# Optimization experiments

Measured on AMD Instinct MI355X. Metric: run time of the kernel, lower is better.

Reference implementation:

```python
import jax, jax.numpy as jnp
import numpy as np

B, N, E, H = 4, 2048, 256, 8
D = E // H
EPS = 1e-5


def _layernorm(x, g, b):
    mu = jnp.mean(x, axis=-1, keepdims=True)
    var = jnp.mean(jnp.square(x - mu), axis=-1, keepdims=True)
    return (x - mu) * jax.lax.rsqrt(var + EPS) * g + b


def setup_inputs() -> dict:
    key = jax.random.key(0)
    ks = jax.random.split(key, 8)
    s = 1.0 / np.sqrt(E)
    lin = lambda k: (jax.random.normal(k, (E, E), jnp.float32) * s)
    return {
        "x_l": jax.random.normal(ks[0], (B, N, E), jnp.float32),
        "x_r": jax.random.normal(ks[1], (B, N, E), jnp.float32),
        "Wq": lin(ks[2]), "bq": jnp.zeros((E,), jnp.float32),
        "Wk": lin(ks[3]), "bk": jnp.zeros((E,), jnp.float32),
        "Wv": lin(ks[4]), "bv": jnp.zeros((E,), jnp.float32),
        "Wp": lin(ks[5]), "bp": jnp.zeros((E,), jnp.float32),
        "ln_g": jnp.ones((E,), jnp.float32), "ln_b": jnp.zeros((E,), jnp.float32),
        "rn_g": jnp.ones((E,), jnp.float32), "rn_b": jnp.zeros((E,), jnp.float32),
    }


def reference(x_l, x_r, Wq, bq, Wk, bk, Wv, bv, Wp, bp, ln_g, ln_b, rn_g, rn_b):
    # projections -> [b, h, n, d]
    q = (x_l @ Wq + bq).reshape(B, N, H, D).transpose(0, 2, 1, 3)
    k = (x_r @ Wk + bk).reshape(B, N, H, D).transpose(0, 2, 1, 3)
    # shared value from the difference of the two streams
    v = ((x_l - x_r) @ Wv + bv).reshape(B, N, H, D).transpose(0, 2, 1, 3)

    energy = jnp.einsum('bhqd,bhkd->bhqk', q, k)  # [b,h,n,n]
    attn = jax.nn.softmax(energy / np.sqrt(D), axis=-1)  # dropout p=0 (eval)

    # attn used as-is and transposed against the SAME value tensor
    out_l = jnp.einsum('bhqk,bhkd->bhqd', attn, v)
    out_r = jnp.einsum('bhqk,bhqd->bhkd', attn, v)  # == attn^T @ v

    out_l = out_l.transpose(0, 2, 1, 3).reshape(B, N, E)
    out_r = out_r.transpose(0, 2, 1, 3).reshape(B, N, E)

    out_l = _layernorm(out_l @ Wp + bp, ln_g, ln_b) + x_l
    out_r = _layernorm(out_r @ Wp + bp, rn_g, rn_b) + x_r
    return (out_l, out_r)
```

## Files before the change

kernel.cpp:

```cpp
#include <hip/hip_runtime.h>
#include <math.h>


typedef __attribute__((ext_vector_type(8))) short short8;
typedef __attribute__((ext_vector_type(4))) float f32x4;
typedef __attribute__((ext_vector_type(16))) float f32x16;
typedef __attribute__((ext_vector_type(4))) unsigned short u16x4;

union FragU { unsigned int u[4]; short8 s8; };

__device__ __forceinline__ unsigned short bf16_rn(float f) {
    union { float f; unsigned int u; } c; c.f = f;
    return (unsigned short)((c.u + 0x7FFFu + ((c.u >> 16) & 1u)) >> 16);
}
__device__ __forceinline__ float b2f(unsigned short u) {
    union { unsigned int i; float f; } c; c.i = ((unsigned int)u) << 16;
    return c.f;
}

#if __has_builtin(__builtin_amdgcn_exp2f)
__device__ __forceinline__ float fexp2(float x) { return __builtin_amdgcn_exp2f(x); }
#else
__device__ __forceinline__ float fexp2(float x) { return exp2f(x); }
#endif

__device__ __forceinline__ f32x4 mfma16(short8 a, short8 b, f32x4 c) {
    return __builtin_amdgcn_mfma_f32_16x16x32_bf16(a, b, c, 0, 0, 0);
}
__device__ __forceinline__ f32x16 mfma32(short8 a, short8 b, f32x16 c) {
    return __builtin_amdgcn_mfma_f32_32x32x16_bf16(a, b, c, 0, 0, 0);
}

__device__ __forceinline__ void plswap(unsigned int& x, unsigned int& y) {
    asm("v_permlane32_swap_b32 %0, %1" : "+v"(x), "+v"(y));
}

__device__ __forceinline__ short8 pfrag(unsigned int w0, unsigned int w1,
                                        unsigned int w2, unsigned int w3) {
    plswap(w0, w2);
    plswap(w1, w3);
    FragU fu;
    fu.u[0] = w0; fu.u[1] = w1; fu.u[2] = w2; fu.u[3] = w3;
    return fu.s8;
}

__global__ void prep_all(const float* __restrict__ xl, const float* __restrict__ xr,
                         const float* __restrict__ Wq, const float* __restrict__ Wk,
                         const float* __restrict__ Wv, const float* __restrict__ Wp,
                         unsigned short* __restrict__ xlb, unsigned short* __restrict__ xrb,
                         unsigned short* __restrict__ xdb,
                         unsigned short* __restrict__ Wqt, unsigned short* __restrict__ Wkt,
                         unsigned short* __restrict__ Wvt, unsigned short* __restrict__ Wpt) {
    const int bid = blockIdx.x;
    if (bid < 2048) {
        const size_t i = ((size_t)bid * 256 + threadIdx.x) * 4;
        const float4 A = *(const float4*)(xl + i);
        const float4 Bv = *(const float4*)(xr + i);
        u16x4 pa = { bf16_rn(A.x), bf16_rn(A.y), bf16_rn(A.z), bf16_rn(A.w) };
        u16x4 pb = { bf16_rn(Bv.x), bf16_rn(Bv.y), bf16_rn(Bv.z), bf16_rn(Bv.w) };
        u16x4 pd = { bf16_rn(A.x - Bv.x), bf16_rn(A.y - Bv.y),
                     bf16_rn(A.z - Bv.z), bf16_rn(A.w - Bv.w) };
        *(u16x4*)(xlb + i) = pa;
        *(u16x4*)(xrb + i) = pb;
        *(u16x4*)(xdb + i) = pd;
    } else {
        const int gid = (bid - 2048) * 256 + threadIdx.x;
        const int m = gid >> 16;
        const int idx = gid & 65535;
        const int k = idx >> 8, n = idx & 255;
        const float* W = (m == 0) ? Wq : (m == 1) ? Wk : (m == 2) ? Wv : Wp;
        unsigned short* Wt = (m == 0) ? Wqt : (m == 1) ? Wkt : (m == 2) ? Wvt : Wpt;
        Wt[n * 256 + k] = bf16_rn(W[(size_t)k * 256 + n]);
    }
}

__launch_bounds__(256)
__global__ void qkv_gemm(const unsigned short* __restrict__ xlb,
                         const unsigned short* __restrict__ xrb,
                         const unsigned short* __restrict__ xdb,
                         const unsigned short* __restrict__ Wqt,
                         const unsigned short* __restrict__ Wkt,
                         const unsigned short* __restrict__ Wvt,
                         const float* __restrict__ bq, const float* __restrict__ bk,
                         const float* __restrict__ bv,
                         unsigned short* __restrict__ Qg, unsigned short* __restrict__ Kg,
                         unsigned short* __restrict__ Vtg) {
    const int z = blockIdx.z;
    const unsigned short* A  = (z == 0) ? xlb : (z == 1) ? xrb : xdb;
    const unsigned short* Wt = (z == 0) ? Wqt : (z == 1) ? Wkt : Wvt;
    const float* bias        = (z == 0) ? bq  : (z == 1) ? bk  : bv;

    __shared__ unsigned short At[2][128][40];
    __shared__ unsigned short Bt[2][64][40];

    const int tid = threadIdx.x;
    const int lane = tid & 63, wv = tid >> 6;
    const int a = lane & 15, g = lane >> 4;
    const int wr = wv >> 1, wc = wv & 1;
    const int r0 = blockIdx.x * 128;
    const int c0 = blockIdx.y * 64;

    const f32x4 fz = {0.f, 0.f, 0.f, 0.f};
    f32x4 acc[4][2];
#pragma unroll
    for (int f = 0; f < 4; ++f)
#pragma unroll
        for (int t = 0; t < 2; ++t) acc[f][t] = fz;

    const int arow = tid >> 1, aoff = (tid & 1) * 16;
    const int brow = tid >> 2, boff = (tid & 3) * 8;
    const unsigned short* asrc = A + (size_t)(r0 + arow) * 256 + aoff;
    const unsigned short* bsrc = Wt + (size_t)(c0 + brow) * 256 + boff;

#define QKV_STAGE(KS, BUF)                                                      \
    {                                                                           \
        *(short8*)&At[BUF][arow][aoff]     = *(const short8*)(asrc + (KS) * 32); \
        *(short8*)&At[BUF][arow][aoff + 8] = *(const short8*)(asrc + (KS) * 32 + 8); \
        *(short8*)&Bt[BUF][brow][boff]     = *(const short8*)(bsrc + (KS) * 32); \
    }

    QKV_STAGE(0, 0)
    __syncthreads();

#pragma unroll
    for (int ks = 0; ks < 8; ++ks) {
        const int b = ks & 1;
        if (ks < 7) QKV_STAGE(ks + 1, b ^ 1)
        short8 af[4], bfr[2];
#pragma unroll
        for (int f = 0; f < 4; ++f) af[f] = *(const short8*)&At[b][wr * 64 + f * 16 + a][g * 8];
#pragma unroll
        for (int t = 0; t < 2; ++t) bfr[t] = *(const short8*)&Bt[b][wc * 32 + t * 16 + a][g * 8];
#pragma unroll
        for (int f = 0; f < 4; ++f)
#pragma unroll
            for (int t = 0; t < 2; ++t) acc[f][t] = mfma16(af[f], bfr[t], acc[f][t]);
        __syncthreads();
    }
#undef QKV_STAGE

    const float scq = 0.17677669529663687f * 1.4426950408889634f;
#pragma unroll
    for (int t = 0; t < 2; ++t) {
        const int C = c0 + wc * 32 + t * 16 + a;
        const float bb = bias[C];
        const int h = C >> 5, d = C & 31;
#pragma unroll
        for (int f = 0; f < 4; ++f) {
            const int Rb = r0 + wr * 64 + f * 16 + g * 4;
            const int b_ = Rb >> 11, n = Rb & 2047;
            const int bhh = b_ * 8 + h;
            float v[4];
#pragma unroll
            for (int r = 0; r < 4; ++r) {
                v[r] = acc[f][t][r] + bb;
                if (z == 0) v[r] *= scq;
            }
            if (z < 2) {
                unsigned short* dst = ((z == 0) ? Qg : Kg) + (size_t)(bhh * 2048 + n) * 32 + d;
#pragma unroll
                for (int r = 0; r < 4; ++r) dst[(size_t)r * 32] = bf16_rn(v[r]);
            } else {
                u16x4 pk = { bf16_rn(v[0]), bf16_rn(v[1]), bf16_rn(v[2]), bf16_rn(v[3]) };
                *(u16x4*)(Vtg + (size_t)(bhh * 32 + d) * 2048 + n) = pk;
            }
        }
    }
}

#define P1_TILE(SB)                                                             \
    {                                                                           \
        const short8 ck0 = *(const short8*)((SB) + ro);                         \
        const short8 ck1 = *(const short8*)((SB) + 512 + ro);                   \
        const short8 cv0 = *(const short8*)((SB) + 1024 + ro);                  \
        const short8 cv1 = *(const short8*)((SB) + 1536 + ro);                  \
        f32x16 s = {};                                                          \
        s = mfma32(ck0, qf0, s);                                                \
        s = mfma32(ck1, qf1, s);                                                \
        float p[16];                                                            \
        _Pragma("unroll") for (int j = 0; j < 16; ++j) p[j] = fexp2(s[j]);      \
        l_run += (((p[0] + p[1]) + (p[2] + p[3])) + ((p[4] + p[5]) + (p[6] + p[7]))) \
               + (((p[8] + p[9]) + (p[10] + p[11])) + ((p[12] + p[13]) + (p[14] + p[15]))); \
        unsigned int w[8];                                                      \
        _Pragma("unroll") for (int mm = 0; mm < 8; ++mm)                        \
            asm("v_cvt_pk_bf16_f32 %0, %1, %2"                                  \
                : "=v"(w[mm]) : "v"(p[2 * mm]), "v"(p[2 * mm + 1]));            \
        acc = mfma32(cv0, pfrag(w[0], w[1], w[2], w[3]), acc);                  \
        acc = mfma32(cv1, pfrag(w[4], w[5], w[6], w[7]), acc);                  \
    }

__launch_bounds__(512, 4)
__global__ void attn_pass1(const unsigned short* __restrict__ Qg,
                           const unsigned short* __restrict__ Kg,
                           const unsigned short* __restrict__ Vtg,
                           unsigned short* __restrict__ AOl,
                           unsigned short* __restrict__ Vsg) {
    __shared__ unsigned short ST[2][2][2][2][2][64][8];
    __shared__ float lsumS[4][64];

    float (*accS)[16][64] = (float (*)[16][64])&ST[0][0][0][0][0][0][0];

    const int f = blockIdx.x;
    const int bh = 4 * (f & 7) + (f >> 7);
    const int qblk = (f >> 3) & 15;
    const int tid = threadIdx.x;
    const int wv = tid >> 6;
    const int qi = wv & 3, z = wv >> 2;
    const int lane = tid & 63, l31 = lane & 31, hi = lane >> 5;
    const int q0 = qblk * 128 + qi * 32;

    const unsigned short* Qb = Qg + (size_t)bh * 2048 * 32;
    const unsigned short* Kb = Kg + (size_t)bh * 2048 * 32;
    const unsigned short* Vb = Vtg + (size_t)bh * 32 * 2048;

    const short8 qf0 = *(const short8*)(Qb + (size_t)(q0 + l31) * 32 + hi * 8);
    const short8 qf1 = *(const short8*)(Qb + (size_t)(q0 + l31) * 32 + 16 + hi * 8);

    const int kv = qi >> 1;
    const int srow = (qi & 1) * 16 + (lane >> 2);
    const int m = lane & 3;
    unsigned short* wp00 = &ST[z][0][0][kv][m >> 1][srow + 32 * (m & 1)][0];
    unsigned short* wp01 = &ST[z][0][1][kv][m >> 1][srow + 32 * (m & 1)][0];
    unsigned short* wp10 = &ST[z][1][0][kv][m >> 1][srow + 32 * (m & 1)][0];
    unsigned short* wp11 = &ST[z][1][1][kv][m >> 1][srow + 32 * (m & 1)][0];
    const size_t gstep = kv ? 32 : 1024;
    const unsigned short* sgb = kv
        ? Vb + (size_t)srow * 2048 + m * 8
        : Kb + (size_t)srow * 32 + m * 8;
    const int zt = z * 32;

    const unsigned short* rb00 = &ST[z][0][0][0][0][0][0];
    const unsigned short* rb01 = &ST[z][0][1][0][0][0][0];
    const unsigned short* rb10 = &ST[z][1][0][0][0][0][0];
    const unsigned short* rb11 = &ST[z][1][1][0][0][0][0];
    const int ro = (l31 + 32 * hi) * 8;

    f32x16 acc = {};
    float l_run = 0.f;

    short8 rr0 = *(const short8*)(sgb + (size_t)(zt + 0) * gstep);
    short8 rr1 = *(const short8*)(sgb + (size_t)(zt + 1) * gstep);
    *(short8*)wp00 = rr0;
    *(short8*)wp01 = rr1;
    rr0 = *(const short8*)(sgb + (size_t)(zt + 2) * gstep);
    rr1 = *(const short8*)(sgb + (size_t)(zt + 3) * gstep);
    __syncthreads();

#pragma unroll
    for (int ph = 0; ph < 16; ++ph) {
        const int pb = ph & 1;
        unsigned short* wA = pb ? wp00 : wp10;
        unsigned short* wB = pb ? wp01 : wp11;
        const unsigned short* rA = pb ? rb10 : rb00;
        const unsigned short* rB = pb ? rb11 : rb01;
        if (ph < 15) { *(short8*)wA = rr0; *(short8*)wB = rr1; }
        if (ph < 14) {
            rr0 = *(const short8*)(sgb + (size_t)(zt + 2 * ph + 4) * gstep);
            rr1 = *(const short8*)(sgb + (size_t)(zt + 2 * ph + 5) * gstep);
        }
        P1_TILE(rA)
        P1_TILE(rB)
        __syncthreads();
    }

    float lsum = l_run + __shfl_xor(l_run, 32);

    if (z == 1) {
#pragma unroll
        for (int j = 0; j < 16; ++j) accS[qi][j][lane] = acc[j];
        lsumS[qi][lane] = lsum;
    }
    __syncthreads();
    if (z == 0) {
        lsum += lsumS[qi][lane];
        const float rl = 1.0f / lsum;
#pragma unroll
        for (int j = 0; j < 16; ++j) acc[j] += accS[qi][j][lane];

        const int b_ = bh >> 3, h = bh & 7;
        const int q = q0 + l31;
        unsigned short* dst = AOl + (size_t)(b_ * 2048 + q) * 256 + h * 32;
#pragma unroll
        for (int g2 = 0; g2 < 4; ++g2) {
            u16x4 pk = { bf16_rn(acc[4 * g2 + 0] * rl), bf16_rn(acc[4 * g2 + 1] * rl),
                         bf16_rn(acc[4 * g2 + 2] * rl), bf16_rn(acc[4 * g2 + 3] * rl) };
            *(u16x4*)(dst + 8 * g2 + 4 * hi) = pk;
        }
        if (hi == 0) lsumS[qi][l31] = rl;
    }
    __syncthreads();
    if (z == 1) {
        const int cb = hi * 16;
        float il[16];
#pragma unroll
        for (int e = 0; e < 16; e += 4) {
            const float4 v4 = *(const float4*)&lsumS[qi][cb + e];
            il[e] = v4.x; il[e + 1] = v4.y; il[e + 2] = v4.z; il[e + 3] = v4.w;
        }
        const unsigned short* vsrc = Vb + (size_t)l31 * 2048 + q0 + cb;
        unsigned short* vdst = Vsg + (size_t)bh * 32 * 2048 + (size_t)l31 * 2048 + q0 + cb;
#pragma unroll
        for (int c4 = 0; c4 < 4; ++c4) {
            const u16x4 vv = *(const u16x4*)(vsrc + c4 * 4);
            u16x4 o = { bf16_rn(b2f(vv.x) * il[c4 * 4 + 0]),
                        bf16_rn(b2f(vv.y) * il[c4 * 4 + 1]),
                        bf16_rn(b2f(vv.z) * il[c4 * 4 + 2]),
                        bf16_rn(b2f(vv.w) * il[c4 * 4 + 3]) };
            *(u16x4*)(vdst + c4 * 4) = o;
        }
    }
}

#define P2_TILE(SB)                                                             \
    {                                                                           \
        const short8 cq0 = *(const short8*)((SB) + ro);                         \
        const short8 cq1 = *(const short8*)((SB) + 512 + ro);                   \
        const short8 cv0 = *(const short8*)((SB) + 1024 + ro);                  \
        const short8 cv1 = *(const short8*)((SB) + 1536 + ro);                  \
        f32x16 s = {};                                                          \
        s = mfma32(cq0, kf0, s);                                                \
        s = mfma32(cq1, kf1, s);                                                \
        float p[16];                                                            \
        _Pragma("unroll") for (int j = 0; j < 16; ++j) p[j] = fexp2(s[j]);      \
        unsigned int w[8];                                                      \
        _Pragma("unroll") for (int mm = 0; mm < 8; ++mm)                        \
            asm("v_cvt_pk_bf16_f32 %0, %1, %2"                                  \
                : "=v"(w[mm]) : "v"(p[2 * mm]), "v"(p[2 * mm + 1]));            \
        acc = mfma32(pfrag(w[0], w[1], w[2], w[3]), cv0, acc);                  \
        acc = mfma32(pfrag(w[4], w[5], w[6], w[7]), cv1, acc);                  \
    }

__launch_bounds__(512, 4)
__global__ void attn_pass2(const unsigned short* __restrict__ Qg,
                           const unsigned short* __restrict__ Kg,
                           const unsigned short* __restrict__ Vsg,
                           unsigned short* __restrict__ AOr) {
    __shared__ unsigned short ST[2][2][2][2][2][64][8];

    float (*accS)[16][64] = (float (*)[16][64])&ST[0][0][0][0][0][0][0];

    const int f = blockIdx.x;
    const int bh = 4 * (f & 7) + (f >> 7);
    const int kblk = (f >> 3) & 15;
    const int tid = threadIdx.x;
    const int wv = tid >> 6;
    const int ki = wv & 3, z = wv >> 2;
    const int lane = tid & 63, l31 = lane & 31, hi = lane >> 5;
    const int k0 = kblk * 128 + ki * 32;

    const unsigned short* Qb = Qg + (size_t)bh * 2048 * 32;
    const unsigned short* Kb = Kg + (size_t)bh * 2048 * 32;
    const unsigned short* Vb = Vsg + (size_t)bh * 32 * 2048;

    const short8 kf0 = *(const short8*)(Kb + (size_t)(k0 + l31) * 32 + hi * 8);
    const short8 kf1 = *(const short8*)(Kb + (size_t)(k0 + l31) * 32 + 16 + hi * 8);

    const int kv = ki >> 1;
    const int srow = (ki & 1) * 16 + (lane >> 2);
    const int m = lane & 3;
    unsigned short* wp00 = &ST[z][0][0][kv][m >> 1][srow + 32 * (m & 1)][0];
    unsigned short* wp01 = &ST[z][0][1][kv][m >> 1][srow + 32 * (m & 1)][0];
    unsigned short* wp10 = &ST[z][1][0][kv][m >> 1][srow + 32 * (m & 1)][0];
    unsigned short* wp11 = &ST[z][1][1][kv][m >> 1][srow + 32 * (m & 1)][0];
    const size_t gstep = kv ? 32 : 1024;
    const unsigned short* sgb = kv
        ? Vb + (size_t)srow * 2048 + m * 8
        : Qb + (size_t)srow * 32 + m * 8;
    const int zt = z * 32;

    const unsigned short* rb00 = &ST[z][0][0][0][0][0][0];
    const unsigned short* rb01 = &ST[z][0][1][0][0][0][0];
    const unsigned short* rb10 = &ST[z][1][0][0][0][0][0];
    const unsigned short* rb11 = &ST[z][1][1][0][0][0][0];
    const int ro = (l31 + 32 * hi) * 8;

    f32x16 acc = {};

    short8 rr0 = *(const short8*)(sgb + (size_t)(zt + 0) * gstep);
    short8 rr1 = *(const short8*)(sgb + (size_t)(zt + 1) * gstep);
    *(short8*)wp00 = rr0;
    *(short8*)wp01 = rr1;
    rr0 = *(const short8*)(sgb + (size_t)(zt + 2) * gstep);
    rr1 = *(const short8*)(sgb + (size_t)(zt + 3) * gstep);
    __syncthreads();

#pragma unroll
    for (int ph = 0; ph < 16; ++ph) {
        const int pb = ph & 1;
        unsigned short* wA = pb ? wp00 : wp10;
        unsigned short* wB = pb ? wp01 : wp11;
        const unsigned short* rA = pb ? rb10 : rb00;
        const unsigned short* rB = pb ? rb11 : rb01;
        if (ph < 15) { *(short8*)wA = rr0; *(short8*)wB = rr1; }
        if (ph < 14) {
            rr0 = *(const short8*)(sgb + (size_t)(zt + 2 * ph + 4) * gstep);
            rr1 = *(const short8*)(sgb + (size_t)(zt + 2 * ph + 5) * gstep);
        }
        P2_TILE(rA)
        P2_TILE(rB)
        __syncthreads();
    }

    if (z == 1) {
#pragma unroll
        for (int j = 0; j < 16; ++j) accS[ki][j][lane] = acc[j];
    }
    __syncthreads();
    if (z == 0) {
#pragma unroll
        for (int j = 0; j < 16; ++j) acc[j] += accS[ki][j][lane];

        const int b_ = bh >> 3, h = bh & 7;
#pragma unroll
        for (int j = 0; j < 16; ++j) {
            const int krow = k0 + (j & 3) + 8 * (j >> 2) + 4 * hi;
            AOr[(size_t)(b_ * 2048 + krow) * 256 + h * 32 + l31] = bf16_rn(acc[j]);
        }
    }
}

__launch_bounds__(256)
__global__ void proj_ln(const unsigned short* __restrict__ AOl,
                        const unsigned short* __restrict__ AOr,
                        const unsigned short* __restrict__ Wpt,
                        const float* __restrict__ bp,
                        const float* __restrict__ ln_g, const float* __restrict__ ln_b,
                        const float* __restrict__ rn_g, const float* __restrict__ rn_b,
                        const float* __restrict__ xl, const float* __restrict__ xr,
                        float* __restrict__ out) {
    __shared__ unsigned short At[32][264];
    __shared__ unsigned short Bt[2][256][40];
    __shared__ float lnS[2][2][2][16];

    const int sel = blockIdx.y;
    const unsigned short* AO = sel ? AOr : AOl;
    const float* gamma = sel ? rn_g : ln_g;
    const float* beta  = sel ? rn_b : ln_b;
    const float* xres  = sel ? xr : xl;
    float* o = out + (size_t)sel * 8192 * 256;

    const int tid = threadIdx.x;
    const int lane = tid & 63, wv = tid >> 6;
    const int a = lane & 15, g = lane >> 4;
    const int wr = wv >> 1, wc = wv & 1;
    const int r0 = blockIdx.x * 32;

    {
        const int row = tid >> 3, seg = (tid & 7) * 32;
        const unsigned short* src = AO + (size_t)(r0 + row) * 256 + seg;
#pragma unroll
        for (int i = 0; i < 4; ++i)
            *(short8*)&At[row][seg + i * 8] = *(const short8*)(src + i * 8);
    }
    const unsigned short* wsrc = Wpt + (size_t)tid * 256;
#pragma unroll
    for (int i = 0; i < 4; ++i)
        *(short8*)&Bt[0][tid][i * 8] = *(const short8*)(wsrc + i * 8);

    const f32x4 fz = {0.f, 0.f, 0.f, 0.f};
    f32x4 acc[8];
#pragma unroll
    for (int cf = 0; cf < 8; ++cf) acc[cf] = fz;

    __syncthreads();

#pragma unroll
    for (int ks = 0; ks < 8; ++ks) {
        const int b = ks & 1;
        if (ks < 7) {
#pragma unroll
            for (int i = 0; i < 4; ++i)
                *(short8*)&Bt[b ^ 1][tid][i * 8] =
                    *(const short8*)(wsrc + (ks + 1) * 32 + i * 8);
        }
        const short8 af = *(const short8*)&At[wr * 16 + a][ks * 32 + g * 8];
#pragma unroll
        for (int cf = 0; cf < 8; ++cf) {
            const short8 bfr = *(const short8*)&Bt[b][wc * 128 + cf * 16 + a][g * 8];
            acc[cf] = mfma16(af, bfr, acc[cf]);
        }
        __syncthreads();
    }

    float bb[8], gg[8], be[8];
#pragma unroll
    for (int cf = 0; cf < 8; ++cf) {
        const int c = wc * 128 + cf * 16 + a;
        bb[cf] = bp[c]; gg[cf] = gamma[c]; be[cf] = beta[c];
    }

    float y[4][8], s1r[4], s2r[4];
#pragma unroll
    for (int r = 0; r < 4; ++r) {
        float s1 = 0.f, s2 = 0.f;
#pragma unroll
        for (int cf = 0; cf < 8; ++cf) {
            const float yv = acc[cf][r] + bb[cf];
            y[r][cf] = yv;
            s1 += yv;
            s2 += yv * yv;
        }
#pragma unroll
        for (int mask = 1; mask <= 8; mask <<= 1) {
            s1 += __shfl_xor(s1, mask);
            s2 += __shfl_xor(s2, mask);
        }
        s1r[r] = s1; s2r[r] = s2;
    }
    if (a == 0) {
#pragma unroll
        for (int r = 0; r < 4; ++r) {
            lnS[wr][wc][0][g * 4 + r] = s1r[r];
            lnS[wr][wc][1][g * 4 + r] = s2r[r];
        }
    }
    __syncthreads();
#pragma unroll
    for (int r = 0; r < 4; ++r) {
        const float s1 = s1r[r] + lnS[wr][wc ^ 1][0][g * 4 + r];
        const float s2 = s2r[r] + lnS[wr][wc ^ 1][1][g * 4 + r];
        const float mu = s1 * (1.0f / 256.0f);
        const float var = s2 * (1.0f / 256.0f) - mu * mu;
        const float rstd = rsqrtf(var + 1e-5f);
        const int R = r0 + wr * 16 + g * 4 + r;
#pragma unroll
        for (int cf = 0; cf < 8; ++cf) {
            const int c = wc * 128 + cf * 16 + a;
            o[(size_t)R * 256 + c] =
                (y[r][cf] - mu) * rstd * gg[cf] + be[cf] + xres[(size_t)R * 256 + c];
        }
    }
}

extern "C" void kernel_launch(void* const* d_in, const int* in_sizes, int n_in,
                              void* d_out, int out_size, void* d_ws, size_t ws_size,
                              hipStream_t stream) {
    const float* x_l  = (const float*)d_in[0];
    const float* x_r  = (const float*)d_in[1];
    const float* Wq   = (const float*)d_in[2];
    const float* bq   = (const float*)d_in[3];
    const float* Wk   = (const float*)d_in[4];
    const float* bk   = (const float*)d_in[5];
    const float* Wv   = (const float*)d_in[6];
    const float* bv   = (const float*)d_in[7];
    const float* Wp   = (const float*)d_in[8];
    const float* bp   = (const float*)d_in[9];
    const float* ln_g = (const float*)d_in[10];
    const float* ln_b = (const float*)d_in[11];
    const float* rn_g = (const float*)d_in[12];
    const float* rn_b = (const float*)d_in[13];

    const size_t SZ_TOK = (size_t)8192 * 256;

    unsigned short* xl_bf = (unsigned short*)d_ws;
    unsigned short* xr_bf = xl_bf + SZ_TOK;
    unsigned short* xd_bf = xr_bf + SZ_TOK;
    unsigned short* Qg    = xd_bf + SZ_TOK;
    unsigned short* Kg    = Qg + SZ_TOK;
    unsigned short* Vtg   = Kg + SZ_TOK;
    unsigned short* Wqt   = Vtg + SZ_TOK;
    unsigned short* Wkt   = Wqt + 65536;
    unsigned short* Wvt   = Wkt + 65536;
    unsigned short* Wpt   = Wvt + 65536;
    unsigned short* AOl   = xl_bf;
    unsigned short* AOr   = xr_bf;
    unsigned short* Vs    = xd_bf;
    float* out = (float*)d_out;

    prep_all<<<3072, 256, 0, stream>>>(x_l, x_r, Wq, Wk, Wv, Wp,
                                       xl_bf, xr_bf, xd_bf, Wqt, Wkt, Wvt, Wpt);
    qkv_gemm<<<dim3(64, 4, 3), 256, 0, stream>>>(xl_bf, xr_bf, xd_bf,
                                                 Wqt, Wkt, Wvt, bq, bk, bv, Qg, Kg, Vtg);
    attn_pass1<<<512, 512, 0, stream>>>(Qg, Kg, Vtg, AOl, Vs);
    attn_pass2<<<512, 512, 0, stream>>>(Qg, Kg, Vs, AOr);
    proj_ln<<<dim3(256, 2), 256, 0, stream>>>(AOl, AOr, Wpt, bp,
                                              ln_g, ln_b, rn_g, rn_b, x_l, x_r, out);
}
```

Baseline: 88.03 us.

## Halve attention block size to 4 waves with 64-row tiles and twice the blocks

Both attention passes now launch 1024 blocks of 256 threads, each covering a 64-row query or key tile with 2 row-waves times 2 KV-split waves, instead of 512 blocks of 512 threads covering 128 rows. The shared staging of K/Q and V tiles is reworked so each thread loads two 16-byte chunks per row, since fewer threads now fill the same LDS tile. The intent is better load balance and occupancy across CUs with smaller workgroups. In exchange each K/V tile staged in LDS is reused by fewer query rows, which raises global and LDS traffic per unit of work.

```diff
diff --git a/kernel.cpp b/kernel.cpp
--- a/kernel.cpp
+++ b/kernel.cpp
@@ -189,25 +189,25 @@
         acc = mfma32(cv1, pfrag(w[4], w[5], w[6], w[7]), acc);                  \
     }
 
-__launch_bounds__(512, 4)
+__launch_bounds__(256, 4)
 __global__ void attn_pass1(const unsigned short* __restrict__ Qg,
                            const unsigned short* __restrict__ Kg,
                            const unsigned short* __restrict__ Vtg,
                            unsigned short* __restrict__ AOl,
                            unsigned short* __restrict__ Vsg) {
     __shared__ unsigned short ST[2][2][2][2][2][64][8];
-    __shared__ float lsumS[4][64];
+    __shared__ float lsumS[2][64];
 
     float (*accS)[16][64] = (float (*)[16][64])&ST[0][0][0][0][0][0][0];
 
     const int f = blockIdx.x;
-    const int bh = 4 * (f & 7) + (f >> 7);
-    const int qblk = (f >> 3) & 15;
+    const int bh = 4 * (f & 7) + (f >> 8);
+    const int qblk = (f >> 3) & 31;
     const int tid = threadIdx.x;
     const int wv = tid >> 6;
-    const int qi = wv & 3, z = wv >> 2;
+    const int qi = wv & 1, z = wv >> 1;
     const int lane = tid & 63, l31 = lane & 31, hi = lane >> 5;
-    const int q0 = qblk * 128 + qi * 32;
+    const int q0 = qblk * 64 + qi * 32;
 
     const unsigned short* Qb = Qg + (size_t)bh * 2048 * 32;
     const unsigned short* Kb = Kg + (size_t)bh * 2048 * 32;
@@ -216,17 +216,17 @@
     const short8 qf0 = *(const short8*)(Qb + (size_t)(q0 + l31) * 32 + hi * 8);
     const short8 qf1 = *(const short8*)(Qb + (size_t)(q0 + l31) * 32 + 16 + hi * 8);
 
-    const int kv = qi >> 1;
-    const int srow = (qi & 1) * 16 + (lane >> 2);
-    const int m = lane & 3;
-    unsigned short* wp00 = &ST[z][0][0][kv][m >> 1][srow + 32 * (m & 1)][0];
-    unsigned short* wp01 = &ST[z][0][1][kv][m >> 1][srow + 32 * (m & 1)][0];
-    unsigned short* wp10 = &ST[z][1][0][kv][m >> 1][srow + 32 * (m & 1)][0];
-    unsigned short* wp11 = &ST[z][1][1][kv][m >> 1][srow + 32 * (m & 1)][0];
+    const int kv = qi;
+    const int srow = lane >> 1;
+    const int m01 = lane & 1;
+    unsigned short* wp00 = &ST[z][0][0][kv][m01][srow][0];
+    unsigned short* wp01 = &ST[z][0][1][kv][m01][srow][0];
+    unsigned short* wp10 = &ST[z][1][0][kv][m01][srow][0];
+    unsigned short* wp11 = &ST[z][1][1][kv][m01][srow][0];
     const size_t gstep = kv ? 32 : 1024;
     const unsigned short* sgb = kv
-        ? Vb + (size_t)srow * 2048 + m * 8
-        : Kb + (size_t)srow * 32 + m * 8;
+        ? Vb + (size_t)srow * 2048 + m01 * 16
+        : Kb + (size_t)srow * 32 + m01 * 16;
     const int zt = z * 32;
 
     const unsigned short* rb00 = &ST[z][0][0][0][0][0][0];
@@ -238,12 +238,16 @@
     f32x16 acc = {};
     float l_run = 0.f;
 
-    short8 rr0 = *(const short8*)(sgb + (size_t)(zt + 0) * gstep);
-    short8 rr1 = *(const short8*)(sgb + (size_t)(zt + 1) * gstep);
-    *(short8*)wp00 = rr0;
-    *(short8*)wp01 = rr1;
-    rr0 = *(const short8*)(sgb + (size_t)(zt + 2) * gstep);
-    rr1 = *(const short8*)(sgb + (size_t)(zt + 3) * gstep);
+    short8 ra0 = *(const short8*)(sgb + (size_t)(zt + 0) * gstep);
+    short8 ra1 = *(const short8*)(sgb + (size_t)(zt + 0) * gstep + 8);
+    short8 rc0 = *(const short8*)(sgb + (size_t)(zt + 1) * gstep);
+    short8 rc1 = *(const short8*)(sgb + (size_t)(zt + 1) * gstep + 8);
+    *(short8*)wp00 = ra0; *(short8*)(wp00 + 256) = ra1;
+    *(short8*)wp01 = rc0; *(short8*)(wp01 + 256) = rc1;
+    ra0 = *(const short8*)(sgb + (size_t)(zt + 2) * gstep);
+    ra1 = *(const short8*)(sgb + (size_t)(zt + 2) * gstep + 8);
+    rc0 = *(const short8*)(sgb + (size_t)(zt + 3) * gstep);
+    rc1 = *(const short8*)(sgb + (size_t)(zt + 3) * gstep + 8);
     __syncthreads();
 
 #pragma unroll
@@ -253,10 +257,15 @@
         unsigned short* wB = pb ? wp01 : wp11;
         const unsigned short* rA = pb ? rb10 : rb00;
         const unsigned short* rB = pb ? rb11 : rb01;
-        if (ph < 15) { *(short8*)wA = rr0; *(short8*)wB = rr1; }
+        if (ph < 15) {
+            *(short8*)wA = ra0; *(short8*)(wA + 256) = ra1;
+            *(short8*)wB = rc0; *(short8*)(wB + 256) = rc1;
+        }
         if (ph < 14) {
-            rr0 = *(const short8*)(sgb + (size_t)(zt + 2 * ph + 4) * gstep);
-            rr1 = *(const short8*)(sgb + (size_t)(zt + 2 * ph + 5) * gstep);
+            ra0 = *(const short8*)(sgb + (size_t)(zt + 2 * ph + 4) * gstep);
+            ra1 = *(const short8*)(sgb + (size_t)(zt + 2 * ph + 4) * gstep + 8);
+            rc0 = *(const short8*)(sgb + (size_t)(zt + 2 * ph + 5) * gstep);
+            rc1 = *(const short8*)(sgb + (size_t)(zt + 2 * ph + 5) * gstep + 8);
         }
         P1_TILE(rA)
         P1_TILE(rB)
@@ -330,7 +339,7 @@
         acc = mfma32(pfrag(w[4], w[5], w[6], w[7]), cv1, acc);                  \
     }
 
-__launch_bounds__(512, 4)
+__launch_bounds__(256, 4)
 __global__ void attn_pass2(const unsigned short* __restrict__ Qg,
                            const unsigned short* __restrict__ Kg,
                            const unsigned short* __restrict__ Vsg,
@@ -340,13 +349,13 @@
     float (*accS)[16][64] = (float (*)[16][64])&ST[0][0][0][0][0][0][0];
 
     const int f = blockIdx.x;
-    const int bh = 4 * (f & 7) + (f >> 7);
-    const int kblk = (f >> 3) & 15;
+    const int bh = 4 * (f & 7) + (f >> 8);
+    const int kblk = (f >> 3) & 31;
     const int tid = threadIdx.x;
     const int wv = tid >> 6;
-    const int ki = wv & 3, z = wv >> 2;
+    const int ki = wv & 1, z = wv >> 1;
     const int lane = tid & 63, l31 = lane & 31, hi = lane >> 5;
-    const int k0 = kblk * 128 + ki * 32;
+    const int k0 = kblk * 64 + ki * 32;
 
     const unsigned short* Qb = Qg + (size_t)bh * 2048 * 32;
     const unsigned short* Kb = Kg + (size_t)bh * 2048 * 32;
@@ -355,17 +364,17 @@
     const short8 kf0 = *(const short8*)(Kb + (size_t)(k0 + l31) * 32 + hi * 8);
     const short8 kf1 = *(const short8*)(Kb + (size_t)(k0 + l31) * 32 + 16 + hi * 8);
 
-    const int kv = ki >> 1;
-    const int srow = (ki & 1) * 16 + (lane >> 2);
-    const int m = lane & 3;
-    unsigned short* wp00 = &ST[z][0][0][kv][m >> 1][srow + 32 * (m & 1)][0];
-    unsigned short* wp01 = &ST[z][0][1][kv][m >> 1][srow + 32 * (m & 1)][0];
-    unsigned short* wp10 = &ST[z][1][0][kv][m >> 1][srow + 32 * (m & 1)][0];
-    unsigned short* wp11 = &ST[z][1][1][kv][m >> 1][srow + 32 * (m & 1)][0];
+    const int kv = ki;
+    const int srow = lane >> 1;
+    const int m01 = lane & 1;
+    unsigned short* wp00 = &ST[z][0][0][kv][m01][srow][0];
+    unsigned short* wp01 = &ST[z][0][1][kv][m01][srow][0];
+    unsigned short* wp10 = &ST[z][1][0][kv][m01][srow][0];
+    unsigned short* wp11 = &ST[z][1][1][kv][m01][srow][0];
     const size_t gstep = kv ? 32 : 1024;
     const unsigned short* sgb = kv
-        ? Vb + (size_t)srow * 2048 + m * 8
-        : Qb + (size_t)srow * 32 + m * 8;
+        ? Vb + (size_t)srow * 2048 + m01 * 16
+        : Qb + (size_t)srow * 32 + m01 * 16;
     const int zt = z * 32;
 
     const unsigned short* rb00 = &ST[z][0][0][0][0][0][0];
@@ -376,12 +385,16 @@
 
     f32x16 acc = {};
 
-    short8 rr0 = *(const short8*)(sgb + (size_t)(zt + 0) * gstep);
-    short8 rr1 = *(const short8*)(sgb + (size_t)(zt + 1) * gstep);
-    *(short8*)wp00 = rr0;
-    *(short8*)wp01 = rr1;
-    rr0 = *(const short8*)(sgb + (size_t)(zt + 2) * gstep);
-    rr1 = *(const short8*)(sgb + (size_t)(zt + 3) * gstep);
+    short8 ra0 = *(const short8*)(sgb + (size_t)(zt + 0) * gstep);
+    short8 ra1 = *(const short8*)(sgb + (size_t)(zt + 0) * gstep + 8);
+    short8 rc0 = *(const short8*)(sgb + (size_t)(zt + 1) * gstep);
+    short8 rc1 = *(const short8*)(sgb + (size_t)(zt + 1) * gstep + 8);
+    *(short8*)wp00 = ra0; *(short8*)(wp00 + 256) = ra1;
+    *(short8*)wp01 = rc0; *(short8*)(wp01 + 256) = rc1;
+    ra0 = *(const short8*)(sgb + (size_t)(zt + 2) * gstep);
+    ra1 = *(const short8*)(sgb + (size_t)(zt + 2) * gstep + 8);
+    rc0 = *(const short8*)(sgb + (size_t)(zt + 3) * gstep);
+    rc1 = *(const short8*)(sgb + (size_t)(zt + 3) * gstep + 8);
     __syncthreads();
 
 #pragma unroll
@@ -391,10 +404,15 @@
         unsigned short* wB = pb ? wp01 : wp11;
         const unsigned short* rA = pb ? rb10 : rb00;
         const unsigned short* rB = pb ? rb11 : rb01;
-        if (ph < 15) { *(short8*)wA = rr0; *(short8*)wB = rr1; }
+        if (ph < 15) {
+            *(short8*)wA = ra0; *(short8*)(wA + 256) = ra1;
+            *(short8*)wB = rc0; *(short8*)(wB + 256) = rc1;
+        }
         if (ph < 14) {
-            rr0 = *(const short8*)(sgb + (size_t)(zt + 2 * ph + 4) * gstep);
-            rr1 = *(const short8*)(sgb + (size_t)(zt + 2 * ph + 5) * gstep);
+            ra0 = *(const short8*)(sgb + (size_t)(zt + 2 * ph + 4) * gstep);
+            ra1 = *(const short8*)(sgb + (size_t)(zt + 2 * ph + 4) * gstep + 8);
+            rc0 = *(const short8*)(sgb + (size_t)(zt + 2 * ph + 5) * gstep);
+            rc1 = *(const short8*)(sgb + (size_t)(zt + 2 * ph + 5) * gstep + 8);
         }
         P2_TILE(rA)
         P2_TILE(rB)
@@ -571,8 +589,8 @@
                                        xl_bf, xr_bf, xd_bf, Wqt, Wkt, Wvt, Wpt);
     qkv_gemm<<<dim3(64, 4, 3), 256, 0, stream>>>(xl_bf, xr_bf, xd_bf,
                                                  Wqt, Wkt, Wvt, bq, bk, bv, Qg, Kg, Vtg);
-    attn_pass1<<<512, 512, 0, stream>>>(Qg, Kg, Vtg, AOl, Vs);
-    attn_pass2<<<512, 512, 0, stream>>>(Qg, Kg, Vs, AOr);
+    attn_pass1<<<1024, 256, 0, stream>>>(Qg, Kg, Vtg, AOl, Vs);
+    attn_pass2<<<1024, 256, 0, stream>>>(Qg, Kg, Vs, AOr);
     proj_ln<<<dim3(256, 2), 256, 0, stream>>>(AOl, AOr, Wpt, bp,
                                               ln_g, ln_b, rn_g, rn_b, x_l, x_r, out);
 }
```

After: 92.99 us. 5.6% more time.
